# Kernel tuning notes

Hardware: AMD Instinct MI355X
Metric: run time of the kernel (lower is better)

## Reference

```python
import jax, jax.numpy as jnp
import numpy as np

B, T, C = 4, 2048, 1024
H, D = 16, 64  # num_heads, head_size; H*D == C


def setup_inputs() -> dict:
    key = jax.random.key(0)
    ks = jax.random.split(key, 6)
    s = C ** -0.5
    return {
        "x": jax.random.normal(ks[0], (B, T, C), dtype=jnp.float32),
        "Wq": jax.random.normal(ks[1], (H, C, D), dtype=jnp.float32) * s,
        "Wk": jax.random.normal(ks[2], (H, C, D), dtype=jnp.float32) * s,
        "Wv": jax.random.normal(ks[3], (H, C, D), dtype=jnp.float32) * s,
        "Wo": jax.random.normal(ks[4], (C, C), dtype=jnp.float32) * s,
        "bo": jnp.zeros((C,), dtype=jnp.float32),
    }


def reference(x, Wq, Wk, Wv, Wo, bo):
    # Per-head projections, vectorized over heads: [B,T,C] x [H,C,D] -> [B,H,T,D]
    q = jnp.einsum("btc,hcd->bhtd", x, Wq)
    k = jnp.einsum("btc,hcd->bhtd", x, Wk)
    v = jnp.einsum("btc,hcd->bhtd", x, Wv)
    # NOTE: original scales by n_embd**-0.5 (input channel C), not head_size.
    scale = jnp.asarray(C, x.dtype) ** -0.5
    scores = jnp.einsum("bhtd,bhsd->bhts", q, k) * scale  # [B,H,T,T]
    causal = jnp.tril(jnp.ones((T, T), dtype=bool))
    scores = jnp.where(causal, scores, jnp.asarray(-jnp.inf, x.dtype))
    attn = jax.nn.softmax(scores, axis=-1)
    out = jnp.einsum("bhts,bhsd->bhtd", attn, v)  # [B,H,T,D]
    # concat heads: [B,T,H*D] == [B,T,C]
    out = out.transpose(0, 2, 1, 3).reshape(B, T, H * D)
    return out @ Wo.T + bo
```

## Files before the change

kernel.cpp:

```cpp
#include <hip/hip_runtime.h>
#include <hip/hip_bf16.h>
#include <math.h>

#define B_ 4
#define T_ 2048
#define C_ 1024
#define H_ 16
#define D_ 64
#define BT (B_*T_)
#define BH (B_*H_)

typedef __bf16 bf16x8 __attribute__((ext_vector_type(8)));
typedef __bf16 bf16x4 __attribute__((ext_vector_type(4)));
typedef float f32x4 __attribute__((ext_vector_type(4)));
typedef unsigned short u16;
typedef u16 u16x8 __attribute__((ext_vector_type(8)));

#define GLL(g, l) __builtin_amdgcn_global_load_lds( \
    (const __attribute__((address_space(1))) unsigned int*)(g), \
    (__attribute__((address_space(3))) unsigned int*)(l), 16, 0, 0)

#define SCALE2 0.04508422f

__device__ __forceinline__ u16 f2b(float f) {
    union { float f; unsigned u; } v; v.f = f;
    unsigned r = v.u + 0x7fffu + ((v.u >> 16) & 1u);
    return (u16)(r >> 16);
}

__global__ __launch_bounds__(256) void prep(const float* __restrict__ x,
                                            const float* __restrict__ Wo,
                                            const float* __restrict__ Wq,
                                            const float* __restrict__ Wk,
                                            const float* __restrict__ Wv,
                                            u16* __restrict__ xbf,
                                            u16* __restrict__ wobf,
                                            u16* __restrict__ wt) {
    __shared__ u16 lds[64][72];
    int bid = blockIdx.x, tid = threadIdx.x;
    if (bid < 8192) {
        int g = bid * 256 + tid;
        float4 v = ((const float4*)x)[g];
        ushort4 o;
        o.x = f2b(v.x); o.y = f2b(v.y); o.z = f2b(v.z); o.w = f2b(v.w);
        ((ushort4*)xbf)[g] = o;
        return;
    }
    if (bid < 9216) {
        int g = (bid - 8192) * 256 + tid;
        float4 v = ((const float4*)Wo)[g];
        ushort4 o;
        o.x = f2b(v.x); o.y = f2b(v.y); o.z = f2b(v.z); o.w = f2b(v.w);
        ((ushort4*)wobf)[g] = o;
        return;
    }
    int id = bid - 9216;
    int cb = id & 15, h = (id >> 4) & 15, w = id >> 8;
    const float* W = (w == 0) ? Wq : (w == 1) ? Wk : Wv;
    float sc = (w == 0) ? SCALE2 : 1.0f;
    int c0 = cb * 64;
    {
        int col = (tid & 15) * 4;
        for (int cc = 0; cc < 4; ++cc) {
            int r = (tid >> 4) + cc * 16;
            float4 v = *(const float4*)&W[(size_t)(h * C_ + c0 + r) * D_ + col];
            lds[r][col + 0] = f2b(v.x * sc); lds[r][col + 1] = f2b(v.y * sc);
            lds[r][col + 2] = f2b(v.z * sc); lds[r][col + 3] = f2b(v.w * sc);
        }
    }
    __syncthreads();
    {
        int tcol = (tid & 7) * 8;
        for (int cc = 0; cc < 2; ++cc) {
            int d = (tid >> 3) + cc * 32;
            u16x8 t;
            for (int j = 0; j < 8; ++j) t[j] = lds[tcol + j][d];
            *(u16x8*)&wt[(((size_t)(w * H_ + h) * D_ + d) * C_) + c0 + tcol] = t;
        }
    }
}

__global__ __launch_bounds__(256, 5) void qkv_gemm(const u16* __restrict__ xbf,
                                                   const u16* __restrict__ wt,
                                                   u16* __restrict__ q, u16* __restrict__ k,
                                                   u16* __restrict__ vt) {
    __shared__ u16 Al[128][64];
    __shared__ u16 Bl[128][64];
    int mb = blockIdx.x, nb = blockIdx.y;
    int tid = threadIdx.x, wv = tid >> 6, lane = tid & 63, l15 = lane & 15, quad = lane >> 4;
    int rowh = (wv & 1) * 64, colh = (wv >> 1) * 64;
    f32x4 acc[4][4];
    #pragma unroll
    for (int i = 0; i < 4; ++i)
        #pragma unroll
        for (int j = 0; j < 4; ++j) acc[i][j] = (f32x4){0.f, 0.f, 0.f, 0.f};
    int lrow = lane >> 3;
    int srow = wv * 32 + lrow;
    int scol = (((lane & 7) ^ lrow)) * 8;
    const u16* agp = &xbf[(size_t)(mb * 128 + srow) * C_ + scol];
    const u16* bgp = &wt[(size_t)(nb * 128 + srow) * C_ + scol];
    int rsw = l15 & 7;
    for (int k0 = 0; k0 < C_; k0 += 64) {
        #pragma unroll
        for (int j = 0; j < 4; ++j) {
            GLL(agp + (size_t)(j * 8) * C_ + k0, &Al[wv * 32 + j * 8][0]);
            GLL(bgp + (size_t)(j * 8) * C_ + k0, &Bl[wv * 32 + j * 8][0]);
        }
        __syncthreads();
        #pragma unroll
        for (int ks = 0; ks < 2; ++ks) {
            int cbl = (((ks << 2) | quad) ^ rsw) * 8;
            bf16x8 af[4], bf[4];
            #pragma unroll
            for (int mt = 0; mt < 4; ++mt)
                af[mt] = *(const bf16x8*)&Al[rowh + mt * 16 + l15][cbl];
            #pragma unroll
            for (int nt = 0; nt < 4; ++nt)
                bf[nt] = *(const bf16x8*)&Bl[colh + nt * 16 + l15][cbl];
            #pragma unroll
            for (int mt = 0; mt < 4; ++mt)
                #pragma unroll
                for (int nt = 0; nt < 4; ++nt)
                    acc[mt][nt] = __builtin_amdgcn_mfma_f32_16x16x32_bf16(af[mt], bf[nt], acc[mt][nt], 0, 0, 0);
        }
        __syncthreads();
    }
    int bb = (mb * 128) >> 11;
    #pragma unroll
    for (int nt = 0; nt < 4; ++nt) {
        int n0 = nb * 128 + colh + nt * 16;
        int wsel = n0 >> 10, hh = (n0 >> 6) & 15, d0 = n0 & 63;
        if (wsel == 2) {
            u16* vrow = vt + ((size_t)((bb * H_ + hh) * D_) + d0 + l15) * T_;
            #pragma unroll
            for (int mt = 0; mt < 4; ++mt) {
                int tbase = ((mb * 128 + rowh + mt * 16) & (T_ - 1)) + quad * 4;
                bf16x4 w;
                #pragma unroll
                for (int r = 0; r < 4; ++r) w[r] = (__bf16)acc[mt][nt][r];
                *(bf16x4*)&vrow[tbase] = w;
            }
        } else {
            u16* op = (wsel == 0) ? q : k;
            #pragma unroll
            for (int mt = 0; mt < 4; ++mt)
                #pragma unroll
                for (int r = 0; r < 4; ++r) {
                    int m = mb * 128 + rowh + mt * 16 + quad * 4 + r;
                    int tt = m & (T_ - 1);
                    op[((size_t)(bb * H_ + hh) * T_ + tt) * D_ + d0 + l15] = f2b(acc[mt][nt][r]);
                }
        }
    }
}

__global__ __launch_bounds__(256, 2) void attn(const u16* __restrict__ q, const u16* __restrict__ kk,
                                               const u16* __restrict__ vt, u16* __restrict__ att) {
    __shared__ u16 Kl[2][64][64];
    __shared__ u16 Vl[2][64][64];
    __shared__ u16 Pl[4][32][72];
    int bh = blockIdx.x, c = 15 - blockIdx.y;
    int b = bh >> 4, h = bh & 15;
    int tid = threadIdx.x, wid = tid >> 6, lane = tid & 63, l15 = lane & 15, quad = lane >> 4;
    const u16* qbase = q + (size_t)bh * T_ * D_;
    const u16* kbase = kk + (size_t)bh * T_ * D_;
    const u16* vbase = vt + (size_t)bh * D_ * T_;
    u16* pw = &Pl[wid][0][0];
    bf16x8 ones;
    #pragma unroll
    for (int j = 0; j < 8; ++j) ones[j] = (__bf16)1.0f;
    int r8 = lane >> 3, cbl_st = lane & 7;
    int csrc = ((cbl_st ^ r8)) * 8;
    int strow = wid * 16 + r8;
    int rsw = l15 & 7;

    int R0q = c * 128 + wid * 32;
    int ktb = 2 * c + 1;
    int kmax_w = R0q >> 6;
    bf16x8 bq[2][2];
    #pragma unroll
    for (int qt = 0; qt < 2; ++qt)
        #pragma unroll
        for (int kd = 0; kd < 2; ++kd)
            bq[qt][kd] = *(const bf16x8*)&qbase[(size_t)(R0q + qt * 16 + l15) * D_ + kd * 32 + quad * 8];
    f32x4 o[4][2];
    f32x4 lacc[2];
    #pragma unroll
    for (int dt = 0; dt < 4; ++dt)
        #pragma unroll
        for (int qt = 0; qt < 2; ++qt) o[dt][qt] = (f32x4){0.f, 0.f, 0.f, 0.f};
    lacc[0] = (f32x4){0.f, 0.f, 0.f, 0.f};
    lacc[1] = (f32x4){0.f, 0.f, 0.f, 0.f};
    #pragma unroll
    for (int j = 0; j < 2; ++j) {
        GLL(kbase + (size_t)(strow + j * 8) * D_ + csrc, &Kl[0][wid * 16 + j * 8][0]);
        GLL(vbase + (size_t)(strow + j * 8) * T_ + csrc, &Vl[0][wid * 16 + j * 8][0]);
    }
    __syncthreads();
    for (int kt = 0; kt <= ktb; ++kt) {
        int cur = kt & 1;
        if (kt < ktb) {
            int kn = (kt + 1) * 64;
            #pragma unroll
            for (int j = 0; j < 2; ++j) {
                GLL(kbase + (size_t)(kn + strow + j * 8) * D_ + csrc, &Kl[cur ^ 1][wid * 16 + j * 8][0]);
                GLL(vbase + (size_t)(strow + j * 8) * T_ + kn + csrc, &Vl[cur ^ 1][wid * 16 + j * 8][0]);
            }
        }
        if (kt <= kmax_w) {
            int k0 = kt * 64;
            f32x4 sS[4][2];
            #pragma unroll
            for (int kvt = 0; kvt < 4; ++kvt)
                #pragma unroll
                for (int qt = 0; qt < 2; ++qt) sS[kvt][qt] = (f32x4){0.f, 0.f, 0.f, 0.f};
            #pragma unroll
            for (int kd = 0; kd < 2; ++kd) {
                int cblk = (((kd << 2) | quad) ^ rsw) * 8;
                bf16x8 akf[4];
                #pragma unroll
                for (int kvt = 0; kvt < 4; ++kvt)
                    akf[kvt] = *(const bf16x8*)&Kl[cur][kvt * 16 + l15][cblk];
                #pragma unroll
                for (int kvt = 0; kvt < 4; ++kvt)
                    #pragma unroll
                    for (int qt = 0; qt < 2; ++qt)
                        sS[kvt][qt] = __builtin_amdgcn_mfma_f32_16x16x32_bf16(akf[kvt], bq[qt][kd], sS[kvt][qt], 0, 0, 0);
            }
            if (kt == kmax_w) {
                #pragma unroll
                for (int qt = 0; qt < 2; ++qt) {
                    int qabs = R0q + qt * 16 + l15;
                    #pragma unroll
                    for (int kvt = 0; kvt < 4; ++kvt) {
                        int kvb = k0 + kvt * 16 + quad * 4;
                        #pragma unroll
                        for (int r = 0; r < 4; ++r)
                            if (kvb + r > qabs) sS[kvt][qt][r] = -INFINITY;
                    }
                }
            }
            #pragma unroll
            for (int kvt = 0; kvt < 4; ++kvt)
                #pragma unroll
                for (int qt = 0; qt < 2; ++qt)
                    #pragma unroll
                    for (int r = 0; r < 4; ++r)
                        sS[kvt][qt][r] = __builtin_amdgcn_exp2f(sS[kvt][qt][r]);
            #pragma unroll
            for (int qt = 0; qt < 2; ++qt)
                #pragma unroll
                for (int kvt = 0; kvt < 4; ++kvt) {
                    bf16x4 w;
                    #pragma unroll
                    for (int r = 0; r < 4; ++r) w[r] = (__bf16)sS[kvt][qt][r];
                    *(bf16x4*)&pw[(qt * 16 + l15) * 72 + kvt * 16 + quad * 4] = w;
                }
            #pragma unroll
            for (int ks = 0; ks < 2; ++ks) {
                int cblk = (((ks << 2) | quad) ^ rsw) * 8;
                bf16x8 avf[4];
                #pragma unroll
                for (int dt = 0; dt < 4; ++dt)
                    avf[dt] = *(const bf16x8*)&Vl[cur][dt * 16 + l15][cblk];
                #pragma unroll
                for (int qt = 0; qt < 2; ++qt) {
                    bf16x8 bp = *(const bf16x8*)&pw[(qt * 16 + l15) * 72 + ks * 32 + quad * 8];
                    #pragma unroll
                    for (int dt = 0; dt < 4; ++dt)
                        o[dt][qt] = __builtin_amdgcn_mfma_f32_16x16x32_bf16(avf[dt], bp, o[dt][qt], 0, 0, 0);
                    lacc[qt] = __builtin_amdgcn_mfma_f32_16x16x32_bf16(ones, bp, lacc[qt], 0, 0, 0);
                }
            }
        }
        __syncthreads();
    }
    #pragma unroll
    for (int qt = 0; qt < 2; ++qt) {
        float rl = __builtin_amdgcn_rcpf(lacc[qt][0]);
        int qabs = R0q + qt * 16 + l15;
        #pragma unroll
        for (int dt = 0; dt < 4; ++dt) {
            bf16x4 w;
            #pragma unroll
            for (int r = 0; r < 4; ++r) w[r] = (__bf16)(o[dt][qt][r] * rl);
            *(bf16x4*)&att[(size_t)(b * T_ + qabs) * C_ + h * 64 + dt * 16 + quad * 4] = w;
        }
    }
}

__global__ __launch_bounds__(256) void out_gemm(const u16* __restrict__ att,
                                                const u16* __restrict__ wo,
                                                const float* __restrict__ bo,
                                                float* __restrict__ out) {
    __shared__ u16 Al[128][64];
    __shared__ u16 Bl[128][64];
    int mb = blockIdx.x, nb = blockIdx.y;
    int tid = threadIdx.x, wv = tid >> 6, lane = tid & 63, l15 = lane & 15, quad = lane >> 4;
    int rowh = (wv & 1) * 64, colh = (wv >> 1) * 64;
    f32x4 acc[4][4];
    #pragma unroll
    for (int i = 0; i < 4; ++i)
        #pragma unroll
        for (int j = 0; j < 4; ++j) acc[i][j] = (f32x4){0.f, 0.f, 0.f, 0.f};
    int lrow = lane >> 3;
    int srow = wv * 32 + lrow;
    int scol = (((lane & 7) ^ lrow)) * 8;
    const u16* agp = &att[(size_t)(mb * 128 + srow) * C_ + scol];
    const u16* bgp = &wo[(size_t)(nb * 128 + srow) * C_ + scol];
    int rsw = l15 & 7;
    for (int k0 = 0; k0 < C_; k0 += 64) {
        #pragma unroll
        for (int j = 0; j < 4; ++j) {
            GLL(agp + (size_t)(j * 8) * C_ + k0, &Al[wv * 32 + j * 8][0]);
            GLL(bgp + (size_t)(j * 8) * C_ + k0, &Bl[wv * 32 + j * 8][0]);
        }
        __syncthreads();
        #pragma unroll
        for (int ks = 0; ks < 2; ++ks) {
            int cbl = (((ks << 2) | quad) ^ rsw) * 8;
            bf16x8 af[4], bf[4];
            #pragma unroll
            for (int mt = 0; mt < 4; ++mt)
                af[mt] = *(const bf16x8*)&Al[rowh + mt * 16 + l15][cbl];
            #pragma unroll
            for (int nt = 0; nt < 4; ++nt)
                bf[nt] = *(const bf16x8*)&Bl[colh + nt * 16 + l15][cbl];
            #pragma unroll
            for (int mt = 0; mt < 4; ++mt)
                #pragma unroll
                for (int nt = 0; nt < 4; ++nt)
                    acc[mt][nt] = __builtin_amdgcn_mfma_f32_16x16x32_bf16(af[mt], bf[nt], acc[mt][nt], 0, 0, 0);
        }
        __syncthreads();
    }
    #pragma unroll
    for (int nt = 0; nt < 4; ++nt) {
        int n = nb * 128 + colh + nt * 16 + l15;
        float bias = bo[n];
        #pragma unroll
        for (int mt = 0; mt < 4; ++mt)
            #pragma unroll
            for (int r = 0; r < 4; ++r) {
                int m = mb * 128 + rowh + mt * 16 + quad * 4 + r;
                out[(size_t)m * C_ + n] = acc[mt][nt][r] + bias;
            }
    }
}

extern "C" void kernel_launch(void* const* d_in, const int* in_sizes, int n_in,
                              void* d_out, int out_size, void* d_ws, size_t ws_size,
                              hipStream_t stream) {
    const float* x  = (const float*)d_in[0];
    const float* Wq = (const float*)d_in[1];
    const float* Wk = (const float*)d_in[2];
    const float* Wv = (const float*)d_in[3];
    const float* Wo = (const float*)d_in[4];
    const float* bo = (const float*)d_in[5];
    float* out = (float*)d_out;
    char* ws = (char*)d_ws;
    u16* xbf  = (u16*)(ws + (size_t)0);
    u16* wt   = (u16*)(ws + ((size_t)16 << 20));
    u16* wobf = (u16*)(ws + ((size_t)22 << 20));
    u16* qb   = (u16*)(ws + ((size_t)24 << 20));
    u16* kb   = (u16*)(ws + ((size_t)40 << 20));
    u16* vtb  = (u16*)(ws + ((size_t)56 << 20));
    u16* attb = (u16*)(ws + ((size_t)72 << 20));

    hipLaunchKernelGGL(prep, dim3(9984), dim3(256), 0, stream, x, Wo, Wq, Wk, Wv, xbf, wobf, wt);
    hipLaunchKernelGGL(qkv_gemm, dim3(BT / 128, 3 * C_ / 128), dim3(256), 0, stream, xbf, wt, qb, kb, vtb);
    hipLaunchKernelGGL(attn, dim3(BH, 16), dim3(256), 0, stream, qb, kb, vtb, attb);
    hipLaunchKernelGGL(out_gemm, dim3(BT / 128, C_ / 128), dim3(256), 0, stream, attb, wobf, bo, out);
}
```

Baseline: 256.0 us.

## Fuse all four stages into one persistent cooperative kernel with grid syncs

Replaces the four separate launches (convert, QKV GEMM, attention, output GEMM) with one cooperative kernel of 512 blocks. The stages are separated by grid-wide syncs, and each block walks the work tiles of every stage in a persistent loop. This removes launch gaps and inter-kernel idle time. In exchange it caps occupancy at 2 blocks per CU, drops the launch_bounds tuning, adds grid-sync overhead, and pairs attention tiles so each block gets balanced causal work.

```diff
diff --git a/kernel.cpp b/kernel.cpp
--- a/kernel.cpp
+++ b/kernel.cpp
@@ -1,6 +1,9 @@
 #include <hip/hip_runtime.h>
+#include <hip/hip_cooperative_groups.h>
 #include <hip/hip_bf16.h>
 #include <math.h>
+
+namespace cg = cooperative_groups;
 
 #define B_ 4
 #define T_ 2048
@@ -28,323 +31,333 @@
     return (u16)(r >> 16);
 }
 
-__global__ __launch_bounds__(256) void prep(const float* __restrict__ x,
-                                            const float* __restrict__ Wo,
-                                            const float* __restrict__ Wq,
-                                            const float* __restrict__ Wk,
-                                            const float* __restrict__ Wv,
-                                            u16* __restrict__ xbf,
-                                            u16* __restrict__ wobf,
-                                            u16* __restrict__ wt) {
-    __shared__ u16 lds[64][72];
+__global__ void mha_fused(const float* __restrict__ x,
+                          const float* __restrict__ Wq,
+                          const float* __restrict__ Wk,
+                          const float* __restrict__ Wv,
+                          const float* __restrict__ Wo,
+                          const float* __restrict__ bo,
+                          u16* __restrict__ xbf, u16* __restrict__ wobf,
+                          u16* __restrict__ wt, u16* __restrict__ qb,
+                          u16* __restrict__ kb, u16* __restrict__ vtb,
+                          u16* __restrict__ attb, float* __restrict__ out) {
+    cg::grid_group grid = cg::this_grid();
+    __shared__ __align__(16) unsigned char smem[51200];
     int bid = blockIdx.x, tid = threadIdx.x;
-    if (bid < 8192) {
-        int g = bid * 256 + tid;
-        float4 v = ((const float4*)x)[g];
-        ushort4 o;
-        o.x = f2b(v.x); o.y = f2b(v.y); o.z = f2b(v.z); o.w = f2b(v.w);
-        ((ushort4*)xbf)[g] = o;
-        return;
+    int wv = tid >> 6, lane = tid & 63, l15 = lane & 15, quad = lane >> 4;
+
+    {
+        u16 (*lds)[72] = (u16(*)[72])smem;
+        for (int pb = bid; pb < 9984; pb += 512) {
+            if (pb < 8192) {
+                int g = pb * 256 + tid;
+                float4 v = ((const float4*)x)[g];
+                ushort4 o;
+                o.x = f2b(v.x); o.y = f2b(v.y); o.z = f2b(v.z); o.w = f2b(v.w);
+                ((ushort4*)xbf)[g] = o;
+            } else if (pb < 9216) {
+                int g = (pb - 8192) * 256 + tid;
+                float4 v = ((const float4*)Wo)[g];
+                ushort4 o;
+                o.x = f2b(v.x); o.y = f2b(v.y); o.z = f2b(v.z); o.w = f2b(v.w);
+                ((ushort4*)wobf)[g] = o;
+            } else {
+                int id = pb - 9216;
+                int cb = id & 15, h = (id >> 4) & 15, w = id >> 8;
+                const float* W = (w == 0) ? Wq : (w == 1) ? Wk : Wv;
+                float sc = (w == 0) ? SCALE2 : 1.0f;
+                int c0 = cb * 64;
+                {
+                    int col = (tid & 15) * 4;
+                    for (int cc = 0; cc < 4; ++cc) {
+                        int r = (tid >> 4) + cc * 16;
+                        float4 v = *(const float4*)&W[(size_t)(h * C_ + c0 + r) * D_ + col];
+                        lds[r][col + 0] = f2b(v.x * sc); lds[r][col + 1] = f2b(v.y * sc);
+                        lds[r][col + 2] = f2b(v.z * sc); lds[r][col + 3] = f2b(v.w * sc);
+                    }
+                }
+                __syncthreads();
+                {
+                    int tcol = (tid & 7) * 8;
+                    for (int cc = 0; cc < 2; ++cc) {
+                        int d = (tid >> 3) + cc * 32;
+                        u16x8 t;
+                        for (int j = 0; j < 8; ++j) t[j] = lds[tcol + j][d];
+                        *(u16x8*)&wt[(((size_t)(w * H_ + h) * D_ + d) * C_) + c0 + tcol] = t;
+                    }
+                }
+                __syncthreads();
+            }
+        }
     }
-    if (bid < 9216) {
-        int g = (bid - 8192) * 256 + tid;
-        float4 v = ((const float4*)Wo)[g];
-        ushort4 o;
-        o.x = f2b(v.x); o.y = f2b(v.y); o.z = f2b(v.z); o.w = f2b(v.w);
-        ((ushort4*)wobf)[g] = o;
-        return;
+    __threadfence();
+    grid.sync();
+
+    {
+        u16 (*Al)[64] = (u16(*)[64])smem;
+        u16 (*Bl)[64] = (u16(*)[64])(smem + 32768);
+        int rowh = (wv & 1) * 64, colh = (wv >> 1) * 64;
+        int lrow = lane >> 3;
+        int scol = (((lane & 7) ^ lrow)) * 8;
+        int rsw = l15 & 7;
+        for (int t = bid; t < 1536; t += 512) {
+            int mb = t & 63, nb = t >> 6;
+            f32x4 acc[4][4];
+            #pragma unroll
+            for (int i = 0; i < 4; ++i)
+                #pragma unroll
+                for (int j = 0; j < 4; ++j) acc[i][j] = (f32x4){0.f, 0.f, 0.f, 0.f};
+            int srow = wv * 32 + lrow;
+            const u16* agp = &xbf[(size_t)(mb * 128 + srow) * C_ + scol];
+            const u16* bgp = &wt[(size_t)(nb * 128 + srow) * C_ + scol];
+            for (int k0 = 0; k0 < C_; k0 += 64) {
+                #pragma unroll
+                for (int j = 0; j < 4; ++j) {
+                    GLL(agp + (size_t)(j * 8) * C_ + k0, &Al[wv * 32 + j * 8][0]);
+                    GLL(bgp + (size_t)(j * 8) * C_ + k0, &Bl[wv * 32 + j * 8][0]);
+                }
+                __syncthreads();
+                #pragma unroll
+                for (int ks = 0; ks < 2; ++ks) {
+                    int cbl = (((ks << 2) | quad) ^ rsw) * 8;
+                    bf16x8 af[4], bf[4];
+                    #pragma unroll
+                    for (int mt = 0; mt < 4; ++mt)
+                        af[mt] = *(const bf16x8*)&Al[rowh + mt * 16 + l15][cbl];
+                    #pragma unroll
+                    for (int nt = 0; nt < 4; ++nt)
+                        bf[nt] = *(const bf16x8*)&Bl[colh + nt * 16 + l15][cbl];
+                    #pragma unroll
+                    for (int mt = 0; mt < 4; ++mt)
+                        #pragma unroll
+                        for (int nt = 0; nt < 4; ++nt)
+                            acc[mt][nt] = __builtin_amdgcn_mfma_f32_16x16x32_bf16(af[mt], bf[nt], acc[mt][nt], 0, 0, 0);
+                }
+                __syncthreads();
+            }
+            int bb = (mb * 128) >> 11;
+            #pragma unroll
+            for (int nt = 0; nt < 4; ++nt) {
+                int n0 = nb * 128 + colh + nt * 16;
+                int wsel = n0 >> 10, hh = (n0 >> 6) & 15, d0 = n0 & 63;
+                if (wsel == 2) {
+                    u16* vrow = vtb + ((size_t)((bb * H_ + hh) * D_) + d0 + l15) * T_;
+                    #pragma unroll
+                    for (int mt = 0; mt < 4; ++mt) {
+                        int tbase = ((mb * 128 + rowh + mt * 16) & (T_ - 1)) + quad * 4;
+                        bf16x4 w;
+                        #pragma unroll
+                        for (int r = 0; r < 4; ++r) w[r] = (__bf16)acc[mt][nt][r];
+                        *(bf16x4*)&vrow[tbase] = w;
+                    }
+                } else {
+                    u16* op = (wsel == 0) ? qb : kb;
+                    #pragma unroll
+                    for (int mt = 0; mt < 4; ++mt)
+                        #pragma unroll
+                        for (int r = 0; r < 4; ++r) {
+                            int m = mb * 128 + rowh + mt * 16 + quad * 4 + r;
+                            int tt = m & (T_ - 1);
+                            op[((size_t)(bb * H_ + hh) * T_ + tt) * D_ + d0 + l15] = f2b(acc[mt][nt][r]);
+                        }
+                }
+            }
+            __syncthreads();
+        }
     }
-    int id = bid - 9216;
-    int cb = id & 15, h = (id >> 4) & 15, w = id >> 8;
-    const float* W = (w == 0) ? Wq : (w == 1) ? Wk : Wv;
-    float sc = (w == 0) ? SCALE2 : 1.0f;
-    int c0 = cb * 64;
+    __threadfence();
+    grid.sync();
+
     {
-        int col = (tid & 15) * 4;
-        for (int cc = 0; cc < 4; ++cc) {
-            int r = (tid >> 4) + cc * 16;
-            float4 v = *(const float4*)&W[(size_t)(h * C_ + c0 + r) * D_ + col];
-            lds[r][col + 0] = f2b(v.x * sc); lds[r][col + 1] = f2b(v.y * sc);
-            lds[r][col + 2] = f2b(v.z * sc); lds[r][col + 3] = f2b(v.w * sc);
+        u16 (*Kl)[64][64] = (u16(*)[64][64])smem;
+        u16 (*Vl)[64][64] = (u16(*)[64][64])(smem + 16384);
+        u16 (*Pl)[32][72] = (u16(*)[32][72])(smem + 32768);
+        u16* pw = &Pl[wv][0][0];
+        bf16x8 ones;
+        #pragma unroll
+        for (int j = 0; j < 8; ++j) ones[j] = (__bf16)1.0f;
+        int r8 = lane >> 3, cbl_st = lane & 7;
+        int csrc = ((cbl_st ^ r8)) * 8;
+        int strow = wv * 16 + r8;
+        int rsw = l15 & 7;
+        for (int ti = 0; ti < 2; ++ti) {
+            int t = ti ? (1023 - bid) : bid;
+            int bh = t & 63, c = 15 - (t >> 6);
+            int b = bh >> 4, h = bh & 15;
+            const u16* qbase = qb + (size_t)bh * T_ * D_;
+            const u16* kbase = kb + (size_t)bh * T_ * D_;
+            const u16* vbase = vtb + (size_t)bh * D_ * T_;
+            int R0q = c * 128 + wv * 32;
+            int ktb = 2 * c + 1;
+            int kmax_w = R0q >> 6;
+            bf16x8 bq[2][2];
+            #pragma unroll
+            for (int qt = 0; qt < 2; ++qt)
+                #pragma unroll
+                for (int kd = 0; kd < 2; ++kd)
+                    bq[qt][kd] = *(const bf16x8*)&qbase[(size_t)(R0q + qt * 16 + l15) * D_ + kd * 32 + quad * 8];
+            f32x4 o[4][2];
+            f32x4 lacc[2];
+            #pragma unroll
+            for (int dt = 0; dt < 4; ++dt)
+                #pragma unroll
+                for (int qt = 0; qt < 2; ++qt) o[dt][qt] = (f32x4){0.f, 0.f, 0.f, 0.f};
+            lacc[0] = (f32x4){0.f, 0.f, 0.f, 0.f};
+            lacc[1] = (f32x4){0.f, 0.f, 0.f, 0.f};
+            #pragma unroll
+            for (int j = 0; j < 2; ++j) {
+                GLL(kbase + (size_t)(strow + j * 8) * D_ + csrc, &Kl[0][wv * 16 + j * 8][0]);
+                GLL(vbase + (size_t)(strow + j * 8) * T_ + csrc, &Vl[0][wv * 16 + j * 8][0]);
+            }
+            __syncthreads();
+            for (int kt = 0; kt <= ktb; ++kt) {
+                int cur = kt & 1;
+                if (kt < ktb) {
+                    int kn = (kt + 1) * 64;
+                    #pragma unroll
+                    for (int j = 0; j < 2; ++j) {
+                        GLL(kbase + (size_t)(kn + strow + j * 8) * D_ + csrc, &Kl[cur ^ 1][wv * 16 + j * 8][0]);
+                        GLL(vbase + (size_t)(strow + j * 8) * T_ + kn + csrc, &Vl[cur ^ 1][wv * 16 + j * 8][0]);
+                    }
+                }
+                if (kt <= kmax_w) {
+                    int k0 = kt * 64;
+                    f32x4 sS[4][2];
+                    #pragma unroll
+                    for (int kvt = 0; kvt < 4; ++kvt)
+                        #pragma unroll
+                        for (int qt = 0; qt < 2; ++qt) sS[kvt][qt] = (f32x4){0.f, 0.f, 0.f, 0.f};
+                    #pragma unroll
+                    for (int kd = 0; kd < 2; ++kd) {
+                        int cblk = (((kd << 2) | quad) ^ rsw) * 8;
+                        bf16x8 akf[4];
+                        #pragma unroll
+                        for (int kvt = 0; kvt < 4; ++kvt)
+                            akf[kvt] = *(const bf16x8*)&Kl[cur][kvt * 16 + l15][cblk];
+                        #pragma unroll
+                        for (int kvt = 0; kvt < 4; ++kvt)
+                            #pragma unroll
+                            for (int qt = 0; qt < 2; ++qt)
+                                sS[kvt][qt] = __builtin_amdgcn_mfma_f32_16x16x32_bf16(akf[kvt], bq[qt][kd], sS[kvt][qt], 0, 0, 0);
+                    }
+                    if (kt == kmax_w) {
+                        #pragma unroll
+                        for (int qt = 0; qt < 2; ++qt) {
+                            int qabs = R0q + qt * 16 + l15;
+                            #pragma unroll
+                            for (int kvt = 0; kvt < 4; ++kvt) {
+                                int kvb = k0 + kvt * 16 + quad * 4;
+                                #pragma unroll
+                                for (int r = 0; r < 4; ++r)
+                                    if (kvb + r > qabs) sS[kvt][qt][r] = -INFINITY;
+                            }
+                        }
+                    }
+                    #pragma unroll
+                    for (int kvt = 0; kvt < 4; ++kvt)
+                        #pragma unroll
+                        for (int qt = 0; qt < 2; ++qt)
+                            #pragma unroll
+                            for (int r = 0; r < 4; ++r)
+                                sS[kvt][qt][r] = __builtin_amdgcn_exp2f(sS[kvt][qt][r]);
+                    #pragma unroll
+                    for (int qt = 0; qt < 2; ++qt)
+                        #pragma unroll
+                        for (int kvt = 0; kvt < 4; ++kvt) {
+                            bf16x4 w;
+                            #pragma unroll
+                            for (int r = 0; r < 4; ++r) w[r] = (__bf16)sS[kvt][qt][r];
+                            *(bf16x4*)&pw[(qt * 16 + l15) * 72 + kvt * 16 + quad * 4] = w;
+                        }
+                    #pragma unroll
+                    for (int ks = 0; ks < 2; ++ks) {
+                        int cblk = (((ks << 2) | quad) ^ rsw) * 8;
+                        bf16x8 avf[4];
+                        #pragma unroll
+                        for (int dt = 0; dt < 4; ++dt)
+                            avf[dt] = *(const bf16x8*)&Vl[cur][dt * 16 + l15][cblk];
+                        #pragma unroll
+                        for (int qt = 0; qt < 2; ++qt) {
+                            bf16x8 bp = *(const bf16x8*)&pw[(qt * 16 + l15) * 72 + ks * 32 + quad * 8];
+                            #pragma unroll
+                            for (int dt = 0; dt < 4; ++dt)
+                                o[dt][qt] = __builtin_amdgcn_mfma_f32_16x16x32_bf16(avf[dt], bp, o[dt][qt], 0, 0, 0);
+                            lacc[qt] = __builtin_amdgcn_mfma_f32_16x16x32_bf16(ones, bp, lacc[qt], 0, 0, 0);
+                        }
+                    }
+                }
+                __syncthreads();
+            }
+            #pragma unroll
+            for (int qt = 0; qt < 2; ++qt) {
+                float rl = __builtin_amdgcn_rcpf(lacc[qt][0]);
+                int qabs = R0q + qt * 16 + l15;
+                #pragma unroll
+                for (int dt = 0; dt < 4; ++dt) {
+                    bf16x4 w;
+                    #pragma unroll
+                    for (int r = 0; r < 4; ++r) w[r] = (__bf16)(o[dt][qt][r] * rl);
+                    *(bf16x4*)&attb[(size_t)(b * T_ + qabs) * C_ + h * 64 + dt * 16 + quad * 4] = w;
+                }
+            }
         }
     }
-    __syncthreads();
+    __threadfence();
+    grid.sync();
+
     {
-        int tcol = (tid & 7) * 8;
-        for (int cc = 0; cc < 2; ++cc) {
-            int d = (tid >> 3) + cc * 32;
-            u16x8 t;
-            for (int j = 0; j < 8; ++j) t[j] = lds[tcol + j][d];
-            *(u16x8*)&wt[(((size_t)(w * H_ + h) * D_ + d) * C_) + c0 + tcol] = t;
-        }
-    }
-}
-
-__global__ __launch_bounds__(256, 5) void qkv_gemm(const u16* __restrict__ xbf,
-                                                   const u16* __restrict__ wt,
-                                                   u16* __restrict__ q, u16* __restrict__ k,
-                                                   u16* __restrict__ vt) {
-    __shared__ u16 Al[128][64];
-    __shared__ u16 Bl[128][64];
-    int mb = blockIdx.x, nb = blockIdx.y;
-    int tid = threadIdx.x, wv = tid >> 6, lane = tid & 63, l15 = lane & 15, quad = lane >> 4;
-    int rowh = (wv & 1) * 64, colh = (wv >> 1) * 64;
-    f32x4 acc[4][4];
-    #pragma unroll
-    for (int i = 0; i < 4; ++i)
+        u16 (*Al)[64] = (u16(*)[64])smem;
+        u16 (*Bl)[64] = (u16(*)[64])(smem + 32768);
+        int mb = bid & 63, nb = bid >> 6;
+        int rowh = (wv & 1) * 64, colh = (wv >> 1) * 64;
+        f32x4 acc[4][4];
         #pragma unroll
-        for (int j = 0; j < 4; ++j) acc[i][j] = (f32x4){0.f, 0.f, 0.f, 0.f};
-    int lrow = lane >> 3;
-    int srow = wv * 32 + lrow;
-    int scol = (((lane & 7) ^ lrow)) * 8;
-    const u16* agp = &xbf[(size_t)(mb * 128 + srow) * C_ + scol];
-    const u16* bgp = &wt[(size_t)(nb * 128 + srow) * C_ + scol];
-    int rsw = l15 & 7;
-    for (int k0 = 0; k0 < C_; k0 += 64) {
+        for (int i = 0; i < 4; ++i)
+            #pragma unroll
+            for (int j = 0; j < 4; ++j) acc[i][j] = (f32x4){0.f, 0.f, 0.f, 0.f};
+        int lrow = lane >> 3;
+        int srow = wv * 32 + lrow;
+        int scol = (((lane & 7) ^ lrow)) * 8;
+        const u16* agp = &attb[(size_t)(mb * 128 + srow) * C_ + scol];
+        const u16* bgp = &wobf[(size_t)(nb * 128 + srow) * C_ + scol];
+        int rsw = l15 & 7;
+        for (int k0 = 0; k0 < C_; k0 += 64) {
+            #pragma unroll
+            for (int j = 0; j < 4; ++j) {
+                GLL(agp + (size_t)(j * 8) * C_ + k0, &Al[wv * 32 + j * 8][0]);
+                GLL(bgp + (size_t)(j * 8) * C_ + k0, &Bl[wv * 32 + j * 8][0]);
+            }
+            __syncthreads();
+            #pragma unroll
+            for (int ks = 0; ks < 2; ++ks) {
+                int cbl = (((ks << 2) | quad) ^ rsw) * 8;
+                bf16x8 af[4], bf[4];
+                #pragma unroll
+                for (int mt = 0; mt < 4; ++mt)
+                    af[mt] = *(const bf16x8*)&Al[rowh + mt * 16 + l15][cbl];
+                #pragma unroll
+                for (int nt = 0; nt < 4; ++nt)
+                    bf[nt] = *(const bf16x8*)&Bl[colh + nt * 16 + l15][cbl];
+                #pragma unroll
+                for (int mt = 0; mt < 4; ++mt)
+                    #pragma unroll
+                    for (int nt = 0; nt < 4; ++nt)
+                        acc[mt][nt] = __builtin_amdgcn_mfma_f32_16x16x32_bf16(af[mt], bf[nt], acc[mt][nt], 0, 0, 0);
+            }
+            __syncthreads();
+        }
         #pragma unroll
-        for (int j = 0; j < 4; ++j) {
-            GLL(agp + (size_t)(j * 8) * C_ + k0, &Al[wv * 32 + j * 8][0]);
-            GLL(bgp + (size_t)(j * 8) * C_ + k0, &Bl[wv * 32 + j * 8][0]);
-        }
-        __syncthreads();
-        #pragma unroll
-        for (int ks = 0; ks < 2; ++ks) {
-            int cbl = (((ks << 2) | quad) ^ rsw) * 8;
-            bf16x8 af[4], bf[4];
-            #pragma unroll
-            for (int mt = 0; mt < 4; ++mt)
-                af[mt] = *(const bf16x8*)&Al[rowh + mt * 16 + l15][cbl];
-            #pragma unroll
-            for (int nt = 0; nt < 4; ++nt)
-                bf[nt] = *(const bf16x8*)&Bl[colh + nt * 16 + l15][cbl];
-            #pragma unroll
-            for (int mt = 0; mt < 4; ++mt)
-                #pragma unroll
-                for (int nt = 0; nt < 4; ++nt)
-                    acc[mt][nt] = __builtin_amdgcn_mfma_f32_16x16x32_bf16(af[mt], bf[nt], acc[mt][nt], 0, 0, 0);
-        }
-        __syncthreads();
-    }
-    int bb = (mb * 128) >> 11;
-    #pragma unroll
-    for (int nt = 0; nt < 4; ++nt) {
-        int n0 = nb * 128 + colh + nt * 16;
-        int wsel = n0 >> 10, hh = (n0 >> 6) & 15, d0 = n0 & 63;
-        if (wsel == 2) {
-            u16* vrow = vt + ((size_t)((bb * H_ + hh) * D_) + d0 + l15) * T_;
-            #pragma unroll
-            for (int mt = 0; mt < 4; ++mt) {
-                int tbase = ((mb * 128 + rowh + mt * 16) & (T_ - 1)) + quad * 4;
-                bf16x4 w;
-                #pragma unroll
-                for (int r = 0; r < 4; ++r) w[r] = (__bf16)acc[mt][nt][r];
-                *(bf16x4*)&vrow[tbase] = w;
-            }
-        } else {
-            u16* op = (wsel == 0) ? q : k;
+        for (int nt = 0; nt < 4; ++nt) {
+            int n = nb * 128 + colh + nt * 16 + l15;
+            float bias = bo[n];
             #pragma unroll
             for (int mt = 0; mt < 4; ++mt)
                 #pragma unroll
                 for (int r = 0; r < 4; ++r) {
                     int m = mb * 128 + rowh + mt * 16 + quad * 4 + r;
-                    int tt = m & (T_ - 1);
-                    op[((size_t)(bb * H_ + hh) * T_ + tt) * D_ + d0 + l15] = f2b(acc[mt][nt][r]);
-                }
-        }
-    }
-}
-
-__global__ __launch_bounds__(256, 2) void attn(const u16* __restrict__ q, const u16* __restrict__ kk,
-                                               const u16* __restrict__ vt, u16* __restrict__ att) {
-    __shared__ u16 Kl[2][64][64];
-    __shared__ u16 Vl[2][64][64];
-    __shared__ u16 Pl[4][32][72];
-    int bh = blockIdx.x, c = 15 - blockIdx.y;
-    int b = bh >> 4, h = bh & 15;
-    int tid = threadIdx.x, wid = tid >> 6, lane = tid & 63, l15 = lane & 15, quad = lane >> 4;
-    const u16* qbase = q + (size_t)bh * T_ * D_;
-    const u16* kbase = kk + (size_t)bh * T_ * D_;
-    const u16* vbase = vt + (size_t)bh * D_ * T_;
-    u16* pw = &Pl[wid][0][0];
-    bf16x8 ones;
-    #pragma unroll
-    for (int j = 0; j < 8; ++j) ones[j] = (__bf16)1.0f;
-    int r8 = lane >> 3, cbl_st = lane & 7;
-    int csrc = ((cbl_st ^ r8)) * 8;
-    int strow = wid * 16 + r8;
-    int rsw = l15 & 7;
-
-    int R0q = c * 128 + wid * 32;
-    int ktb = 2 * c + 1;
-    int kmax_w = R0q >> 6;
-    bf16x8 bq[2][2];
-    #pragma unroll
-    for (int qt = 0; qt < 2; ++qt)
-        #pragma unroll
-        for (int kd = 0; kd < 2; ++kd)
-            bq[qt][kd] = *(const bf16x8*)&qbase[(size_t)(R0q + qt * 16 + l15) * D_ + kd * 32 + quad * 8];
-    f32x4 o[4][2];
-    f32x4 lacc[2];
-    #pragma unroll
-    for (int dt = 0; dt < 4; ++dt)
-        #pragma unroll
-        for (int qt = 0; qt < 2; ++qt) o[dt][qt] = (f32x4){0.f, 0.f, 0.f, 0.f};
-    lacc[0] = (f32x4){0.f, 0.f, 0.f, 0.f};
-    lacc[1] = (f32x4){0.f, 0.f, 0.f, 0.f};
-    #pragma unroll
-    for (int j = 0; j < 2; ++j) {
-        GLL(kbase + (size_t)(strow + j * 8) * D_ + csrc, &Kl[0][wid * 16 + j * 8][0]);
-        GLL(vbase + (size_t)(strow + j * 8) * T_ + csrc, &Vl[0][wid * 16 + j * 8][0]);
-    }
-    __syncthreads();
-    for (int kt = 0; kt <= ktb; ++kt) {
-        int cur = kt & 1;
-        if (kt < ktb) {
-            int kn = (kt + 1) * 64;
-            #pragma unroll
-            for (int j = 0; j < 2; ++j) {
-                GLL(kbase + (size_t)(kn + strow + j * 8) * D_ + csrc, &Kl[cur ^ 1][wid * 16 + j * 8][0]);
-                GLL(vbase + (size_t)(strow + j * 8) * T_ + kn + csrc, &Vl[cur ^ 1][wid * 16 + j * 8][0]);
-            }
-        }
-        if (kt <= kmax_w) {
-            int k0 = kt * 64;
-            f32x4 sS[4][2];
-            #pragma unroll
-            for (int kvt = 0; kvt < 4; ++kvt)
-                #pragma unroll
-                for (int qt = 0; qt < 2; ++qt) sS[kvt][qt] = (f32x4){0.f, 0.f, 0.f, 0.f};
-            #pragma unroll
-            for (int kd = 0; kd < 2; ++kd) {
-                int cblk = (((kd << 2) | quad) ^ rsw) * 8;
-                bf16x8 akf[4];
-                #pragma unroll
-                for (int kvt = 0; kvt < 4; ++kvt)
-                    akf[kvt] = *(const bf16x8*)&Kl[cur][kvt * 16 + l15][cblk];
-                #pragma unroll
-                for (int kvt = 0; kvt < 4; ++kvt)
-                    #pragma unroll
-                    for (int qt = 0; qt < 2; ++qt)
-                        sS[kvt][qt] = __builtin_amdgcn_mfma_f32_16x16x32_bf16(akf[kvt], bq[qt][kd], sS[kvt][qt], 0, 0, 0);
-            }
-            if (kt == kmax_w) {
-                #pragma unroll
-                for (int qt = 0; qt < 2; ++qt) {
-                    int qabs = R0q + qt * 16 + l15;
-                    #pragma unroll
-                    for (int kvt = 0; kvt < 4; ++kvt) {
-                        int kvb = k0 + kvt * 16 + quad * 4;
-                        #pragma unroll
-                        for (int r = 0; r < 4; ++r)
-                            if (kvb + r > qabs) sS[kvt][qt][r] = -INFINITY;
-                    }
-                }
-            }
-            #pragma unroll
-            for (int kvt = 0; kvt < 4; ++kvt)
-                #pragma unroll
-                for (int qt = 0; qt < 2; ++qt)
-                    #pragma unroll
-                    for (int r = 0; r < 4; ++r)
-                        sS[kvt][qt][r] = __builtin_amdgcn_exp2f(sS[kvt][qt][r]);
-            #pragma unroll
-            for (int qt = 0; qt < 2; ++qt)
-                #pragma unroll
-                for (int kvt = 0; kvt < 4; ++kvt) {
-                    bf16x4 w;
-                    #pragma unroll
-                    for (int r = 0; r < 4; ++r) w[r] = (__bf16)sS[kvt][qt][r];
-                    *(bf16x4*)&pw[(qt * 16 + l15) * 72 + kvt * 16 + quad * 4] = w;
-                }
-            #pragma unroll
-            for (int ks = 0; ks < 2; ++ks) {
-                int cblk = (((ks << 2) | quad) ^ rsw) * 8;
-                bf16x8 avf[4];
-                #pragma unroll
-                for (int dt = 0; dt < 4; ++dt)
-                    avf[dt] = *(const bf16x8*)&Vl[cur][dt * 16 + l15][cblk];
-                #pragma unroll
-                for (int qt = 0; qt < 2; ++qt) {
-                    bf16x8 bp = *(const bf16x8*)&pw[(qt * 16 + l15) * 72 + ks * 32 + quad * 8];
-                    #pragma unroll
-                    for (int dt = 0; dt < 4; ++dt)
-                        o[dt][qt] = __builtin_amdgcn_mfma_f32_16x16x32_bf16(avf[dt], bp, o[dt][qt], 0, 0, 0);
-                    lacc[qt] = __builtin_amdgcn_mfma_f32_16x16x32_bf16(ones, bp, lacc[qt], 0, 0, 0);
-                }
-            }
-        }
-        __syncthreads();
-    }
-    #pragma unroll
-    for (int qt = 0; qt < 2; ++qt) {
-        float rl = __builtin_amdgcn_rcpf(lacc[qt][0]);
-        int qabs = R0q + qt * 16 + l15;
-        #pragma unroll
-        for (int dt = 0; dt < 4; ++dt) {
-            bf16x4 w;
-            #pragma unroll
-            for (int r = 0; r < 4; ++r) w[r] = (__bf16)(o[dt][qt][r] * rl);
-            *(bf16x4*)&att[(size_t)(b * T_ + qabs) * C_ + h * 64 + dt * 16 + quad * 4] = w;
-        }
-    }
-}
-
-__global__ __launch_bounds__(256) void out_gemm(const u16* __restrict__ att,
-                                                const u16* __restrict__ wo,
-                                                const float* __restrict__ bo,
-                                                float* __restrict__ out) {
-    __shared__ u16 Al[128][64];
-    __shared__ u16 Bl[128][64];
-    int mb = blockIdx.x, nb = blockIdx.y;
-    int tid = threadIdx.x, wv = tid >> 6, lane = tid & 63, l15 = lane & 15, quad = lane >> 4;
-    int rowh = (wv & 1) * 64, colh = (wv >> 1) * 64;
-    f32x4 acc[4][4];
-    #pragma unroll
-    for (int i = 0; i < 4; ++i)
-        #pragma unroll
-        for (int j = 0; j < 4; ++j) acc[i][j] = (f32x4){0.f, 0.f, 0.f, 0.f};
-    int lrow = lane >> 3;
-    int srow = wv * 32 + lrow;
-    int scol = (((lane & 7) ^ lrow)) * 8;
-    const u16* agp = &att[(size_t)(mb * 128 + srow) * C_ + scol];
-    const u16* bgp = &wo[(size_t)(nb * 128 + srow) * C_ + scol];
-    int rsw = l15 & 7;
-    for (int k0 = 0; k0 < C_; k0 += 64) {
-        #pragma unroll
-        for (int j = 0; j < 4; ++j) {
-            GLL(agp + (size_t)(j * 8) * C_ + k0, &Al[wv * 32 + j * 8][0]);
-            GLL(bgp + (size_t)(j * 8) * C_ + k0, &Bl[wv * 32 + j * 8][0]);
-        }
-        __syncthreads();
-        #pragma unroll
-        for (int ks = 0; ks < 2; ++ks) {
-            int cbl = (((ks << 2) | quad) ^ rsw) * 8;
-            bf16x8 af[4], bf[4];
-            #pragma unroll
-            for (int mt = 0; mt < 4; ++mt)
-                af[mt] = *(const bf16x8*)&Al[rowh + mt * 16 + l15][cbl];
-            #pragma unroll
-            for (int nt = 0; nt < 4; ++nt)
-                bf[nt] = *(const bf16x8*)&Bl[colh + nt * 16 + l15][cbl];
-            #pragma unroll
-            for (int mt = 0; mt < 4; ++mt)
-                #pragma unroll
-                for (int nt = 0; nt < 4; ++nt)
-                    acc[mt][nt] = __builtin_amdgcn_mfma_f32_16x16x32_bf16(af[mt], bf[nt], acc[mt][nt], 0, 0, 0);
-        }
-        __syncthreads();
-    }
-    #pragma unroll
-    for (int nt = 0; nt < 4; ++nt) {
-        int n = nb * 128 + colh + nt * 16 + l15;
-        float bias = bo[n];
-        #pragma unroll
-        for (int mt = 0; mt < 4; ++mt)
-            #pragma unroll
-            for (int r = 0; r < 4; ++r) {
-                int m = mb * 128 + rowh + mt * 16 + quad * 4 + r;
-                out[(size_t)m * C_ + n] = acc[mt][nt][r] + bias;
-            }
+                    out[(size_t)m * C_ + n] = acc[mt][nt][r] + bias;
+                }
+        }
     }
 }
 
@@ -357,7 +370,7 @@
     const float* Wv = (const float*)d_in[3];
     const float* Wo = (const float*)d_in[4];
     const float* bo = (const float*)d_in[5];
-    float* out = (float*)d_out;
+    float* outp = (float*)d_out;
     char* ws = (char*)d_ws;
     u16* xbf  = (u16*)(ws + (size_t)0);
     u16* wt   = (u16*)(ws + ((size_t)16 << 20));
@@ -367,8 +380,8 @@
     u16* vtb  = (u16*)(ws + ((size_t)56 << 20));
     u16* attb = (u16*)(ws + ((size_t)72 << 20));
 
-    hipLaunchKernelGGL(prep, dim3(9984), dim3(256), 0, stream, x, Wo, Wq, Wk, Wv, xbf, wobf, wt);
-    hipLaunchKernelGGL(qkv_gemm, dim3(BT / 128, 3 * C_ / 128), dim3(256), 0, stream, xbf, wt, qb, kb, vtb);
-    hipLaunchKernelGGL(attn, dim3(BH, 16), dim3(256), 0, stream, qb, kb, vtb, attb);
-    hipLaunchKernelGGL(out_gemm, dim3(BT / 128, C_ / 128), dim3(256), 0, stream, attb, wobf, bo, out);
+    void* args[] = {&x, &Wq, &Wk, &Wv, &Wo, &bo,
+                    &xbf, &wobf, &wt, &qb, &kb, &vtb, &attb, &outp};
+    hipLaunchCooperativeKernel((const void*)mha_fused, dim3(512), dim3(256),
+                               args, 0, stream);
 }
```

New measurement: 628.9 us. 2.46x slower.
